# Optimization experiments

Hardware: AMD Instinct MI355X
Metric: run time of the kernel (lower is better)

The kernel has to match this reference:

```python
import jax, jax.numpy as jnp
import numpy as np

N_QUBITS = 4
N_LAYERS = 3
BATCH = 1048576  # 2**20; batched state vector [B, 2,2,2,2] complex64 = 128 MB


def setup_inputs() -> dict:
    key = jax.random.key(0)
    k1, k2 = jax.random.split(key)
    x = jax.random.normal(k1, (BATCH, N_QUBITS), dtype=jnp.float32)
    q_weights = jax.random.normal(k2, (N_LAYERS, N_QUBITS, 3), dtype=jnp.float32) * 0.1
    return {"x": x, "q_weights": q_weights}


def _ry_mat(theta):
    # RY(t) = [[cos t/2, -sin t/2], [sin t/2, cos t/2]]; theta: [] or [B]
    c = jnp.cos(theta * 0.5).astype(jnp.complex64)
    s = jnp.sin(theta * 0.5).astype(jnp.complex64)
    return jnp.stack([jnp.stack([c, -s], -1), jnp.stack([s, c], -1)], -2)


def _rz_mat(theta):
    # RZ(t) = diag(e^{-it/2}, e^{it/2})
    e = jnp.exp(-0.5j * theta.astype(jnp.complex64))
    z = jnp.zeros_like(e)
    return jnp.stack([jnp.stack([e, z], -1), jnp.stack([z, jnp.conj(e)], -1)], -2)


def _apply_1q(state, U, wire):
    # state: [B,2,2,2,2]; U: [2,2] (shared) or [B,2,2] (per-sample)
    ax = wire + 1
    state = jnp.moveaxis(state, ax, -1)
    if U.ndim == 3:
        state = jnp.einsum('b...o,bno->b...n', state, U)
    else:
        state = jnp.einsum('b...o,no->b...n', state, U)
    return jnp.moveaxis(state, -1, ax)


def _cnot(state, c, t):
    # flip target bit on the control=1 slice
    ca, ta = c + 1, t + 1
    s0 = jnp.take(state, 0, axis=ca)
    s1 = jnp.take(state, 1, axis=ca)
    ta2 = ta if ta < ca else ta - 1
    s1 = jnp.flip(s1, axis=ta2)
    return jnp.stack([s0, s1], axis=ca)


def _circuit(x, q_weights):
    B = x.shape[0]
    xn = jnp.tanh(x) * jnp.pi  # [B, 4]
    # |0000>
    state = jnp.zeros((B,) + (2,) * N_QUBITS, dtype=jnp.complex64)
    state = state.at[:, 0, 0, 0, 0].set(1.0 + 0.0j)
    # angle encoding: RY(2x_i) then RZ(x_i), per-sample batched 2x2 gates
    for i in range(N_QUBITS):
        state = _apply_1q(state, _ry_mat(2.0 * xn[:, i]), i)
        state = _apply_1q(state, _rz_mat(xn[:, i]), i)
    # variational layers: Rot(phi,theta,omega) = RZ(omega) @ RY(theta) @ RZ(phi)
    for l in range(N_LAYERS):
        for i in range(N_QUBITS):
            phi, theta, omega = q_weights[l, i, 0], q_weights[l, i, 1], q_weights[l, i, 2]
            U = _rz_mat(omega) @ _ry_mat(theta) @ _rz_mat(phi)
            state = _apply_1q(state, U, i)
        for i in range(N_QUBITS):
            state = _cnot(state, i, (i + 1) % N_QUBITS)
    # <Z_i> = p(bit_i=0) - p(bit_i=1)
    probs = jnp.abs(state) ** 2  # [B,2,2,2,2] real
    evs = []
    for i in range(N_QUBITS):
        axes = tuple(a for a in range(1, N_QUBITS + 1) if a != i + 1)
        marg = jnp.sum(probs, axis=axes)  # [B, 2]
        evs.append(marg[:, 0] - marg[:, 1])
    return jnp.stack(evs, axis=-1).astype(jnp.float32)  # [B, 4]


def reference(x, q_weights):
    return _circuit(x, q_weights)
```

## Files before the change

kernel.cpp:

```cpp
#include <hip/hip_runtime.h>

struct P { float2 re, im; };

__device__ __forceinline__ float2 f2(float x, float y) { return make_float2(x, y); }
__device__ __forceinline__ float2 splat(float s) { return make_float2(s, s); }
__device__ __forceinline__ float2 add2(float2 a, float2 b) { return f2(a.x + b.x, a.y + b.y); }
__device__ __forceinline__ float2 mul2(float2 a, float2 b) { return f2(a.x * b.x, a.y * b.y); }
__device__ __forceinline__ float2 neg2(float2 a) { return f2(-a.x, -a.y); }
__device__ __forceinline__ float2 fma2(float2 a, float2 b, float2 c) {
    return f2(fmaf(a.x, b.x, c.x), fmaf(a.y, b.y, c.y));
}

__device__ __forceinline__ P cmadd2p(float2 u, float2 w, const P& a, const P& b) {
    P r;
    r.re = fma2(splat(u.x), a.re,
           fma2(splat(-u.y), a.im,
           fma2(splat(w.x), b.re, mul2(splat(-w.y), b.im))));
    r.im = fma2(splat(u.x), a.im,
           fma2(splat(u.y), a.re,
           fma2(splat(w.x), b.im, mul2(splat(w.y), b.re))));
    return r;
}

__device__ __forceinline__ P cmulp(const P& a, const P& b) {
    P r;
    r.re = fma2(a.re, b.re, mul2(neg2(a.im), b.im));
    r.im = fma2(a.re, b.im, mul2(a.im, b.re));
    return r;
}

template <int BP>
__device__ __forceinline__ void apply_gate(P st[16], float4 A4, float4 B4) {
    const float2 u00 = f2(A4.x, A4.y), u01 = f2(A4.z, A4.w);
    const float2 u10 = f2(B4.x, B4.y), u11 = f2(B4.z, B4.w);
#pragma unroll
    for (int i = 0; i < 8; i++) {
        const int lo = ((i >> BP) << (BP + 1)) | (i & ((1 << BP) - 1));
        const int hi = lo | (1 << BP);
        const P a = st[lo], b = st[hi];
        st[lo] = cmadd2p(u00, u01, a, b);
        st[hi] = cmadd2p(u10, u11, a, b);
    }
}

template <int CB, int TB>
__device__ __forceinline__ void cnot(P st[16]) {
#pragma unroll
    for (int i = 0; i < 16; i++) {
        if ((i & (1 << CB)) && !(i & (1 << TB))) {
            P t = st[i];
            st[i] = st[i | (1 << TB)];
            st[i | (1 << TB)] = t;
        }
    }
}

struct Enc { float r0, i0, r1, i1; };
__device__ __forceinline__ Enc encode(float xq) {
    const float ax = fabsf(xq);
    const float e  = __builtin_amdgcn_exp2f(ax * -2.8853900817779268f);
    const float r  = __builtin_amdgcn_rcpf(1.0f + e);
    const float t  = copysignf((1.0f - e) * r, xq);
    const float sh = __builtin_amdgcn_sinf(t * 0.25f);
    const float ch = __builtin_amdgcn_cosf(t * 0.25f);
    const float s  = 2.0f * sh * ch;
    const float c  = fmaf(-2.0f * sh, sh, 1.0f);
    return {c * ch, -(c * sh), s * ch, s * sh};
}

__global__ __launch_bounds__(256) void qlayer_kernel(const float* __restrict__ x,
                                                     const float* __restrict__ qw,
                                                     float* __restrict__ out, int B) {
    __shared__ float4 Ug[12][2];
    const int tid = threadIdx.x;
    if (tid < 12) {
        const float phi = qw[tid * 3 + 0];
        const float th  = qw[tid * 3 + 1];
        const float om  = qw[tid * 3 + 2];
        float s, c;   __sincosf(0.5f * th, &s, &c);
        float sa, ca; __sincosf(0.5f * (phi + om), &sa, &ca);
        float sb, cb; __sincosf(0.5f * (phi - om), &sb, &cb);
        Ug[tid][0] = make_float4(c * ca, -c * sa, -s * cb, -s * sb);
        Ug[tid][1] = make_float4(s * cb, -s * sb, c * ca, c * sa);
    }
    __syncthreads();

    const int bA = blockIdx.x * 512 + tid;
    if (bA >= B) return;
    const int bB0 = bA + 256;
    const bool hasB = bB0 < B;
    const int bB = hasB ? bB0 : bA;

    const float4 xA = reinterpret_cast<const float4*>(x)[bA];
    const float4 xB = reinterpret_cast<const float4*>(x)[bB];
    const float xsA[4] = {xA.x, xA.y, xA.z, xA.w};
    const float xsB[4] = {xB.x, xB.y, xB.z, xB.w};

    P v[4][2];
#pragma unroll
    for (int q = 0; q < 4; q++) {
        const Enc eA = encode(xsA[q]);
        const Enc eB = encode(xsB[q]);
        P a; a.re = f2(eA.r0, eB.r0); a.im = f2(eA.i0, eB.i0);
        P b; b.re = f2(eA.r1, eB.r1); b.im = f2(eA.i1, eB.i1);
        const float4 A4 = Ug[q][0], B4 = Ug[q][1];
        v[q][0] = cmadd2p(f2(A4.x, A4.y), f2(A4.z, A4.w), a, b);
        v[q][1] = cmadd2p(f2(B4.x, B4.y), f2(B4.z, B4.w), a, b);
    }

    P t01[4], t23[4];
#pragma unroll
    for (int i = 0; i < 4; i++) {
        t01[i] = cmulp(v[0][(i >> 1) & 1], v[1][i & 1]);
        t23[i] = cmulp(v[2][(i >> 1) & 1], v[3][i & 1]);
    }
    P st[16];
#pragma unroll
    for (int i = 0; i < 16; i++) st[i] = cmulp(t01[i >> 2], t23[i & 3]);

    cnot<3, 2>(st); cnot<2, 1>(st); cnot<1, 0>(st); cnot<0, 3>(st);

    apply_gate<3>(st, Ug[4][0], Ug[4][1]);
    apply_gate<2>(st, Ug[5][0], Ug[5][1]);
    apply_gate<1>(st, Ug[6][0], Ug[6][1]);
    apply_gate<0>(st, Ug[7][0], Ug[7][1]);
    cnot<3, 2>(st); cnot<2, 1>(st); cnot<1, 0>(st); cnot<0, 3>(st);
    apply_gate<3>(st, Ug[8][0], Ug[8][1]);
    apply_gate<2>(st, Ug[9][0], Ug[9][1]);
    apply_gate<1>(st, Ug[10][0], Ug[10][1]);
    apply_gate<0>(st, Ug[11][0], Ug[11][1]);
    cnot<3, 2>(st); cnot<2, 1>(st); cnot<1, 0>(st); cnot<0, 3>(st);

    float2 p[16];
#pragma unroll
    for (int i = 0; i < 16; i++) p[i] = fma2(st[i].re, st[i].re, mul2(st[i].im, st[i].im));

    float2 pr[8];
#pragma unroll
    for (int j = 0; j < 8; j++) pr[j] = add2(p[2 * j], p[2 * j + 1]);

    const float2 s3 = add2(add2(pr[4], pr[5]), add2(pr[6], pr[7]));
    const float2 s2 = add2(add2(pr[2], pr[3]), add2(pr[6], pr[7]));
    const float2 s1 = add2(add2(pr[1], pr[3]), add2(pr[5], pr[7]));
    const float2 s0 = add2(add2(add2(p[1], p[3]), add2(p[5], p[7])),
                           add2(add2(p[9], p[11]), add2(p[13], p[15])));

    float4 evA, evB;
    evA.x = fmaf(-2.0f, s3.x, 1.0f); evB.x = fmaf(-2.0f, s3.y, 1.0f);
    evA.y = fmaf(-2.0f, s2.x, 1.0f); evB.y = fmaf(-2.0f, s2.y, 1.0f);
    evA.z = fmaf(-2.0f, s1.x, 1.0f); evB.z = fmaf(-2.0f, s1.y, 1.0f);
    evA.w = fmaf(-2.0f, s0.x, 1.0f); evB.w = fmaf(-2.0f, s0.y, 1.0f);

    reinterpret_cast<float4*>(out)[bA] = evA;
    if (hasB) reinterpret_cast<float4*>(out)[bB0] = evB;
}

extern "C" void kernel_launch(void* const* d_in, const int* in_sizes, int n_in,
                              void* d_out, int out_size, void* d_ws, size_t ws_size,
                              hipStream_t stream) {
    const float* x  = (const float*)d_in[0];
    const float* qw = (const float*)d_in[1];
    float* out = (float*)d_out;
    const int B = in_sizes[0] / 4;
    const int blocks = (B + 511) / 512;
    qlayer_kernel<<<blocks, 256, 0, stream>>>(x, qw, out, B);
}
```

Measured before the change: 95.86 us.

## Drop packed two-sample float2 math for scalar one-sample-per-thread kernel

Replaces the packed-FP32 scheme, where each thread simulated two batch samples in float2 lanes, with plain scalar complex arithmetic for one sample per thread. The grid doubles to 256 samples per block, and launch bounds now request 8 blocks per CU. The aim is to cut register pressure and raise occupancy, at the cost of giving up the v_pk_fma dual-issue throughput and paying the per-block shared gate setup twice as often.

```diff
diff --git a/kernel.cpp b/kernel.cpp
--- a/kernel.cpp
+++ b/kernel.cpp
@@ -1,54 +1,40 @@
 #include <hip/hip_runtime.h>
 
-struct P { float2 re, im; };
 
-__device__ __forceinline__ float2 f2(float x, float y) { return make_float2(x, y); }
-__device__ __forceinline__ float2 splat(float s) { return make_float2(s, s); }
-__device__ __forceinline__ float2 add2(float2 a, float2 b) { return f2(a.x + b.x, a.y + b.y); }
-__device__ __forceinline__ float2 mul2(float2 a, float2 b) { return f2(a.x * b.x, a.y * b.y); }
-__device__ __forceinline__ float2 neg2(float2 a) { return f2(-a.x, -a.y); }
-__device__ __forceinline__ float2 fma2(float2 a, float2 b, float2 c) {
-    return f2(fmaf(a.x, b.x, c.x), fmaf(a.y, b.y, c.y));
+struct C { float r, i; };
+
+__device__ __forceinline__ C cmul(C a, C b) {
+    C o;
+    o.r = fmaf(a.r, b.r, -(a.i * b.i));
+    o.i = fmaf(a.r, b.i,   a.i * b.r);
+    return o;
 }
 
-__device__ __forceinline__ P cmadd2p(float2 u, float2 w, const P& a, const P& b) {
-    P r;
-    r.re = fma2(splat(u.x), a.re,
-           fma2(splat(-u.y), a.im,
-           fma2(splat(w.x), b.re, mul2(splat(-w.y), b.im))));
-    r.im = fma2(splat(u.x), a.im,
-           fma2(splat(u.y), a.re,
-           fma2(splat(w.x), b.im, mul2(splat(w.y), b.re))));
-    return r;
-}
-
-__device__ __forceinline__ P cmulp(const P& a, const P& b) {
-    P r;
-    r.re = fma2(a.re, b.re, mul2(neg2(a.im), b.im));
-    r.im = fma2(a.re, b.im, mul2(a.im, b.re));
-    return r;
+__device__ __forceinline__ C cmadd(float ur, float ui, float wr, float wi, C a, C b) {
+    C o;
+    o.r = fmaf(ur, a.r, fmaf(-ui, a.i, fmaf(wr, b.r, -(wi * b.i))));
+    o.i = fmaf(ur, a.i, fmaf( ui, a.r, fmaf(wr, b.i,   wi * b.r)));
+    return o;
 }
 
 template <int BP>
-__device__ __forceinline__ void apply_gate(P st[16], float4 A4, float4 B4) {
-    const float2 u00 = f2(A4.x, A4.y), u01 = f2(A4.z, A4.w);
-    const float2 u10 = f2(B4.x, B4.y), u11 = f2(B4.z, B4.w);
+__device__ __forceinline__ void apply_gate(C st[16], float4 A4, float4 B4) {
 #pragma unroll
     for (int i = 0; i < 8; i++) {
         const int lo = ((i >> BP) << (BP + 1)) | (i & ((1 << BP) - 1));
         const int hi = lo | (1 << BP);
-        const P a = st[lo], b = st[hi];
-        st[lo] = cmadd2p(u00, u01, a, b);
-        st[hi] = cmadd2p(u10, u11, a, b);
+        const C a = st[lo], b = st[hi];
+        st[lo] = cmadd(A4.x, A4.y, A4.z, A4.w, a, b);
+        st[hi] = cmadd(B4.x, B4.y, B4.z, B4.w, a, b);
     }
 }
 
 template <int CB, int TB>
-__device__ __forceinline__ void cnot(P st[16]) {
+__device__ __forceinline__ void cnot(C st[16]) {
 #pragma unroll
     for (int i = 0; i < 16; i++) {
         if ((i & (1 << CB)) && !(i & (1 << TB))) {
-            P t = st[i];
+            C t = st[i];
             st[i] = st[i | (1 << TB)];
             st[i | (1 << TB)] = t;
         }
@@ -68,9 +54,9 @@
     return {c * ch, -(c * sh), s * ch, s * sh};
 }
 
-__global__ __launch_bounds__(256) void qlayer_kernel(const float* __restrict__ x,
-                                                     const float* __restrict__ qw,
-                                                     float* __restrict__ out, int B) {
+__global__ __launch_bounds__(256, 8) void qlayer_kernel(const float* __restrict__ x,
+                                                        const float* __restrict__ qw,
+                                                        float* __restrict__ out, int B) {
     __shared__ float4 Ug[12][2];
     const int tid = threadIdx.x;
     if (tid < 12) {
@@ -85,38 +71,31 @@
     }
     __syncthreads();
 
-    const int bA = blockIdx.x * 512 + tid;
-    if (bA >= B) return;
-    const int bB0 = bA + 256;
-    const bool hasB = bB0 < B;
-    const int bB = hasB ? bB0 : bA;
+    const int b = blockIdx.x * 256 + tid;
+    if (b >= B) return;
 
-    const float4 xA = reinterpret_cast<const float4*>(x)[bA];
-    const float4 xB = reinterpret_cast<const float4*>(x)[bB];
-    const float xsA[4] = {xA.x, xA.y, xA.z, xA.w};
-    const float xsB[4] = {xB.x, xB.y, xB.z, xB.w};
+    const float4 xv = reinterpret_cast<const float4*>(x)[b];
+    const float xs[4] = {xv.x, xv.y, xv.z, xv.w};
 
-    P v[4][2];
+    C v[4][2];
 #pragma unroll
     for (int q = 0; q < 4; q++) {
-        const Enc eA = encode(xsA[q]);
-        const Enc eB = encode(xsB[q]);
-        P a; a.re = f2(eA.r0, eB.r0); a.im = f2(eA.i0, eB.i0);
-        P b; b.re = f2(eA.r1, eB.r1); b.im = f2(eA.i1, eB.i1);
+        const Enc e = encode(xs[q]);
+        const C a{e.r0, e.i0}, bv{e.r1, e.i1};
         const float4 A4 = Ug[q][0], B4 = Ug[q][1];
-        v[q][0] = cmadd2p(f2(A4.x, A4.y), f2(A4.z, A4.w), a, b);
-        v[q][1] = cmadd2p(f2(B4.x, B4.y), f2(B4.z, B4.w), a, b);
+        v[q][0] = cmadd(A4.x, A4.y, A4.z, A4.w, a, bv);
+        v[q][1] = cmadd(B4.x, B4.y, B4.z, B4.w, a, bv);
     }
 
-    P t01[4], t23[4];
+    C t01[4], t23[4];
 #pragma unroll
     for (int i = 0; i < 4; i++) {
-        t01[i] = cmulp(v[0][(i >> 1) & 1], v[1][i & 1]);
-        t23[i] = cmulp(v[2][(i >> 1) & 1], v[3][i & 1]);
+        t01[i] = cmul(v[0][(i >> 1) & 1], v[1][i & 1]);
+        t23[i] = cmul(v[2][(i >> 1) & 1], v[3][i & 1]);
     }
-    P st[16];
+    C st[16];
 #pragma unroll
-    for (int i = 0; i < 16; i++) st[i] = cmulp(t01[i >> 2], t23[i & 3]);
+    for (int i = 0; i < 16; i++) st[i] = cmul(t01[i >> 2], t23[i & 3]);
 
     cnot<3, 2>(st); cnot<2, 1>(st); cnot<1, 0>(st); cnot<0, 3>(st);
 
@@ -131,28 +110,25 @@
     apply_gate<0>(st, Ug[11][0], Ug[11][1]);
     cnot<3, 2>(st); cnot<2, 1>(st); cnot<1, 0>(st); cnot<0, 3>(st);
 
-    float2 p[16];
+    float p[16];
 #pragma unroll
-    for (int i = 0; i < 16; i++) p[i] = fma2(st[i].re, st[i].re, mul2(st[i].im, st[i].im));
+    for (int i = 0; i < 16; i++) p[i] = fmaf(st[i].r, st[i].r, st[i].i * st[i].i);
 
-    float2 pr[8];
+    float pr[8];
 #pragma unroll
-    for (int j = 0; j < 8; j++) pr[j] = add2(p[2 * j], p[2 * j + 1]);
+    for (int j = 0; j < 8; j++) pr[j] = p[2 * j] + p[2 * j + 1];
 
-    const float2 s3 = add2(add2(pr[4], pr[5]), add2(pr[6], pr[7]));
-    const float2 s2 = add2(add2(pr[2], pr[3]), add2(pr[6], pr[7]));
-    const float2 s1 = add2(add2(pr[1], pr[3]), add2(pr[5], pr[7]));
-    const float2 s0 = add2(add2(add2(p[1], p[3]), add2(p[5], p[7])),
-                           add2(add2(p[9], p[11]), add2(p[13], p[15])));
+    const float s3 = (pr[4] + pr[5]) + (pr[6] + pr[7]);
+    const float s2 = (pr[2] + pr[3]) + (pr[6] + pr[7]);
+    const float s1 = (pr[1] + pr[3]) + (pr[5] + pr[7]);
+    const float s0 = ((p[1] + p[3]) + (p[5] + p[7])) + ((p[9] + p[11]) + (p[13] + p[15]));
 
-    float4 evA, evB;
-    evA.x = fmaf(-2.0f, s3.x, 1.0f); evB.x = fmaf(-2.0f, s3.y, 1.0f);
-    evA.y = fmaf(-2.0f, s2.x, 1.0f); evB.y = fmaf(-2.0f, s2.y, 1.0f);
-    evA.z = fmaf(-2.0f, s1.x, 1.0f); evB.z = fmaf(-2.0f, s1.y, 1.0f);
-    evA.w = fmaf(-2.0f, s0.x, 1.0f); evB.w = fmaf(-2.0f, s0.y, 1.0f);
-
-    reinterpret_cast<float4*>(out)[bA] = evA;
-    if (hasB) reinterpret_cast<float4*>(out)[bB0] = evB;
+    float4 ev;
+    ev.x = fmaf(-2.0f, s3, 1.0f);
+    ev.y = fmaf(-2.0f, s2, 1.0f);
+    ev.z = fmaf(-2.0f, s1, 1.0f);
+    ev.w = fmaf(-2.0f, s0, 1.0f);
+    reinterpret_cast<float4*>(out)[b] = ev;
 }
 
 extern "C" void kernel_launch(void* const* d_in, const int* in_sizes, int n_in,
@@ -162,6 +138,6 @@
     const float* qw = (const float*)d_in[1];
     float* out = (float*)d_out;
     const int B = in_sizes[0] / 4;
-    const int blocks = (B + 511) / 512;
+    const int blocks = (B + 255) / 256;
     qlayer_kernel<<<blocks, 256, 0, stream>>>(x, qw, out, B);
 }
```

Result: slower. 109.3 us (+14.0%).
